# Kernel tuning notes

Hardware: AMD Instinct MI355X
Metric: run time of the kernel (lower is better)

The kernel has to match this reference:

```python
import jax, jax.numpy as jnp
import numpy as np

B, S, E, D, H = 4, 2048, 512, 64, 8
NEG = float(np.finfo(np.float64).min)  # tf uses tf.float64.min; overflows to -inf in fp32, same softmax effect


def setup_inputs() -> dict:
    key = jax.random.key(0)
    ks = jax.random.split(key, 6)
    std = 0.05  # tf.random_normal_initializer default stddev
    x = jax.random.normal(ks[0], (B, S, E), dtype=jnp.float32)
    Wq = jax.random.normal(ks[1], (H, E, D), dtype=jnp.float32) * std
    Wk = jax.random.normal(ks[2], (H, E, D), dtype=jnp.float32) * std
    Wvd = jax.random.normal(ks[3], (H, E, D), dtype=jnp.float32) * std
    Wvu = jax.random.normal(ks[4], (H, D, E), dtype=jnp.float32) * std
    Wo = jax.random.normal(ks[5], (H, 1), dtype=jnp.float32) * std
    return {"x": x, "Wq": Wq, "Wk": Wk, "Wvd": Wvd, "Wvu": Wvu, "Wo": Wo}


def reference(x, Wq, Wk, Wvd, Wvu, Wo):
    # Per-head projections, vectorized over the head axis h
    Q = jnp.einsum("bse,hed->bhsd", x, Wq)  # [B,H,S,D]
    K = jnp.einsum("bse,hed->bhsd", x, Wk)
    score = jnp.einsum("bhsd,bhtd->bhst", Q, K) / jnp.sqrt(jnp.float32(D))
    # tf.linalg.band_part(score, -1, 0): keep lower triangle (causal)
    tril = jnp.tril(jnp.ones((S, S), dtype=bool))
    score = jnp.where(tril, score, 0.0)
    # tf.where(score != 0, score, float64.min): masks zeros (incl. any exact-zero kept entries)
    score = jnp.where(score != 0, score, jnp.float32(NEG))
    attn = jax.nn.softmax(score, axis=-1)  # [B,H,S,S]
    # low-rank value projection: x @ (Wvdown @ Wvup) per head
    Wv = jnp.einsum("hed,hdf->hef", Wvd, Wvu)  # [H,E,E]
    V = jnp.einsum("bse,hef->bhsf", x, Wv)      # [B,H,S,E]
    heads = jnp.einsum("bhst,bhte->bhse", attn, V)  # [B,H,S,E]
    # stack on last axis then matmul with Wo[H,1] == weighted sum over heads
    out = jnp.einsum("bhse,h->bse", heads, Wo[:, 0])
    return out
```

## Files before the change

### kernel.cpp

```cpp
#include <hip/hip_runtime.h>
#include <math.h>
#include <type_traits>

namespace {
constexpr int B = 4, S = 2048, E = 512, D = 64, H = 8;
constexpr int KD = 512;

typedef short bf8 __attribute__((ext_vector_type(8)));
typedef short bf4 __attribute__((ext_vector_type(4)));
typedef float f4 __attribute__((ext_vector_type(4)));

__device__ __forceinline__ short f2bf(float f) {
  union { float f; unsigned u; } v; v.f = f;
  const unsigned r = v.u + 0x7fffu + ((v.u >> 16) & 1u);
  return (short)(r >> 16);
}

__device__ __forceinline__ unsigned cvt_pk_bf16(float a, float b) {
  unsigned r;
  asm("v_cvt_pk_bf16_f32 %0, %1, %2" : "=v"(r) : "v"(a), "v"(b));
  return r;
}

__device__ __forceinline__ void gload16(const void* g, void* l) {
  __builtin_amdgcn_global_load_lds(
      (const __attribute__((address_space(1))) unsigned int*)g,
      (__attribute__((address_space(3))) unsigned int*)l, 16, 0, 0);
}

__global__ __launch_bounds__(256) void prep_kernel(
    const float* __restrict__ x, const float* __restrict__ Wq,
    const float* __restrict__ Wk, const float* __restrict__ Wvd,
    const float* __restrict__ Wvu, const float* __restrict__ Wo,
    short* __restrict__ xb, short* __restrict__ WcatT,
    short* __restrict__ W2T) {
  __shared__ float T[64][65];
  const int bid = blockIdx.x;
  const int tid = threadIdx.x;
  if (bid < 2048) {
    const size_t i = ((size_t)bid * 256 + tid) * 8;
    const float4 v0 = *(const float4*)(x + i);
    const float4 v1 = *(const float4*)(x + i + 4);
    bf8 o;
    o[0] = f2bf(v0.x); o[1] = f2bf(v0.y); o[2] = f2bf(v0.z); o[3] = f2bf(v0.w);
    o[4] = f2bf(v1.x); o[5] = f2bf(v1.y); o[6] = f2bf(v1.z); o[7] = f2bf(v1.w);
    *(bf8*)(xb + i) = o;
  } else if (bid < 2240) {
    const int r = bid - 2048;
    const int cb = r >> 3, e0 = (r & 7) * 64;
    const int w = cb >> 3, h = cb & 7;
    const float* Wsel = (w == 0) ? Wq : (w == 1) ? Wk : Wvd;
    const float* Wp = Wsel + (size_t)h * E * D;
#pragma unroll
    for (int i = 0; i < 4; ++i) {
      const int f = tid + i * 256;
      const int rr = f >> 4, c4 = f & 15;
      const float4 v = *(const float4*)(Wp + (size_t)(e0 + rr) * D + c4 * 4);
      T[rr][c4 * 4 + 0] = v.x; T[rr][c4 * 4 + 1] = v.y;
      T[rr][c4 * 4 + 2] = v.z; T[rr][c4 * 4 + 3] = v.w;
    }
    __syncthreads();
#pragma unroll
    for (int i = 0; i < 4; ++i) {
      const int f = tid + i * 256;
      const int dr = f >> 4, e4 = f & 15;
      bf4 o;
#pragma unroll
      for (int j = 0; j < 4; ++j) o[j] = f2bf(T[e4 * 4 + j][dr]);
      *(bf4*)(WcatT + (size_t)(cb * 64 + dr) * KD + e0 + e4 * 4) = o;
    }
  } else {
    const int r = bid - 2240;
    const int h = r >> 3, e0 = (r & 7) * 64;
    const float wo = Wo[h];
#pragma unroll
    for (int i = 0; i < 4; ++i) {
      const int f = tid + i * 256;
      const int rr = f >> 4, c4 = f & 15;
      const float4 v = *(const float4*)(Wvu + ((size_t)h * D + rr) * E + e0 + c4 * 4);
      T[rr][c4 * 4 + 0] = v.x * wo; T[rr][c4 * 4 + 1] = v.y * wo;
      T[rr][c4 * 4 + 2] = v.z * wo; T[rr][c4 * 4 + 3] = v.w * wo;
    }
    __syncthreads();
#pragma unroll
    for (int i = 0; i < 4; ++i) {
      const int f = tid + i * 256;
      const int er = f >> 4, d4 = f & 15;
      bf4 o;
#pragma unroll
      for (int j = 0; j < 4; ++j) o[j] = f2bf(T[d4 * 4 + j][er]);
      *(bf4*)(W2T + (size_t)(e0 + er) * KD + h * 64 + d4 * 4) = o;
    }
  }
}

template <int MODE>
__global__ __launch_bounds__(256) void gemm_kernel(
    const short* __restrict__ A, const short* __restrict__ Bt,
    short* __restrict__ Qb, short* __restrict__ Kb, short* __restrict__ Vtg,
    float* __restrict__ Of) {
  const int row0 = blockIdx.x * 128;
  const int ct = blockIdx.y;
  const int tid = threadIdx.x;
  const int w = tid >> 6, l = tid & 63;
  const int wm = w >> 1, wn = w & 1;
  const int lr = l & 15, hi = l >> 4;

  __shared__ short As[128 * 64];
  __shared__ short Bs[128 * 64];

  const short* Ag = A + (size_t)row0 * KD;
  const short* Bg = Bt + (size_t)ct * 128 * KD;

  f4 acc[4][4] = {};
  for (int k0 = 0; k0 < KD; k0 += 64) {
    __syncthreads();
#pragma unroll
    for (int i = 0; i < 4; ++i) {
      const int f = i * 256 + tid;
      const int r = f >> 3, g = f & 7;
      gload16(Ag + (size_t)r * KD + k0 + ((g ^ (r & 7)) << 3), &As[f * 8]);
    }
#pragma unroll
    for (int i = 0; i < 4; ++i) {
      const int f = i * 256 + tid;
      const int r = f >> 3, g = f & 7;
      gload16(Bg + (size_t)r * KD + k0 + ((g ^ (r & 7)) << 3), &Bs[f * 8]);
    }
    __syncthreads();

    bf8 af[4][2], bfv[4][2];
#pragma unroll
    for (int t = 0; t < 4; ++t) {
#pragma unroll
      for (int kh = 0; kh < 2; ++kh) {
        const int ar = wm * 64 + t * 16 + lr;
        af[t][kh] = *(const bf8*)&As[ar * 64 + (((kh * 4 + hi) ^ (ar & 7)) << 3)];
        const int br = wn * 64 + t * 16 + lr;
        bfv[t][kh] = *(const bf8*)&Bs[br * 64 + (((kh * 4 + hi) ^ (br & 7)) << 3)];
      }
    }
#pragma unroll
    for (int mt = 0; mt < 4; ++mt)
#pragma unroll
      for (int nt = 0; nt < 4; ++nt) {
        acc[mt][nt] =
            __builtin_amdgcn_mfma_f32_16x16x32_bf16(af[mt][0], bfv[nt][0], acc[mt][nt], 0, 0, 0);
        acc[mt][nt] =
            __builtin_amdgcn_mfma_f32_16x16x32_bf16(af[mt][1], bfv[nt][1], acc[mt][nt], 0, 0, 0);
      }
  }

  if constexpr (MODE == 0) {
#pragma unroll
    for (int nt = 0; nt < 4; ++nt) {
      const int gc = ct * 128 + wn * 64 + nt * 16 + lr;
      const int cb = gc >> 6, d = gc & 63;
      const int h = cb & 7;
      if (cb < 16) {
        short* Out = (cb < 8) ? Qb : Kb;
#pragma unroll
        for (int mt = 0; mt < 4; ++mt)
#pragma unroll
          for (int reg = 0; reg < 4; ++reg) {
            const int grow = row0 + wm * 64 + mt * 16 + hi * 4 + reg;
            const int b = grow >> 11, s = grow & (S - 1);
            Out[(((size_t)(b * H + h) * S + s) << 6) + d] = f2bf(acc[mt][nt][reg]);
          }
      } else {
#pragma unroll
        for (int mt = 0; mt < 4; ++mt) {
          const int grow0 = row0 + wm * 64 + mt * 16 + hi * 4;
          const int b = grow0 >> 11, s0 = grow0 & (S - 1);
          bf4 o;
#pragma unroll
          for (int reg = 0; reg < 4; ++reg) o[reg] = f2bf(acc[mt][nt][reg]);
          *(bf4*)(Vtg + (((size_t)(b * H + h) * D + d) << 11) + s0) = o;
        }
      }
    }
  } else {
#pragma unroll
    for (int mt = 0; mt < 4; ++mt)
#pragma unroll
      for (int reg = 0; reg < 4; ++reg) {
        const int grow = row0 + wm * 64 + mt * 16 + hi * 4 + reg;
        float* orow = Of + (size_t)grow * 512 + ct * 128 + wn * 64;
#pragma unroll
        for (int nt = 0; nt < 4; ++nt) orow[nt * 16 + lr] = acc[mt][nt][reg];
      }
  }
}

__global__ __launch_bounds__(256) void attn_kernel(
    const short* __restrict__ Qb, const short* __restrict__ Kb,
    const short* __restrict__ Vt, short* __restrict__ PVb) {
  const int bh = blockIdx.x;
  const int qt = (int)(gridDim.y - 1 - blockIdx.y);
  const int b = bh >> 3, h = bh & 7;
  const int tid = threadIdx.x;
  const int w = tid >> 6, l = tid & 63;
  const int lr = l & 15, hi = l >> 4;

  __shared__ short KsA[64 * 64];
  __shared__ short KsB[64 * 64];
  __shared__ short VsA[64 * 64];
  __shared__ short VsB[64 * 64];

  const short* Qg = Qb + ((size_t)bh * S + qt * 64 + w * 16 + lr) * D;
  const bf8 qf0 = *(const bf8*)(Qg + hi * 8);
  const bf8 qf1 = *(const bf8*)(Qg + 32 + hi * 8);

  const short* Kg = Kb + (size_t)bh * S * D;
  const short* Vg = Vt + (size_t)bh * D * S;

  const int sr = tid >> 3, sg = tid & 7;
  const int sswz = (sg ^ (sr & 7)) << 3;
  const int sr2 = sr + 32, sswz2 = (sg ^ (sr2 & 7)) << 3;

  const short* kg0 = Kg + (size_t)sr * D + sswz;
  const short* kg1 = Kg + (size_t)sr2 * D + sswz2;
  const short* vg0 = Vg + (size_t)sr * S + sswz;
  const short* vg1 = Vg + (size_t)sr2 * S + sswz2;

  float lsum4[4] = {};
  f4 accO[4] = {};

  constexpr float LOG2E = 1.44269504088896340736f;
  constexpr float C1 = 0.125f * LOG2E;
  constexpr float C0 = -12.0f * LOG2E;

  auto step = [&](const short* Kl, const short* Vl, auto diag_c) {
    constexpr bool DIAG = decltype(diag_c)::value;
    f4 accS[4] = {};
    __builtin_amdgcn_s_setprio(1);
#pragma unroll
    for (int n = 0; n < 4; ++n) {
      const int tr = n * 16 + lr;
      const bf8 k0 = *(const bf8*)&Kl[tr * 64 + ((hi ^ (tr & 7)) << 3)];
      const bf8 k1 = *(const bf8*)&Kl[tr * 64 + (((4 + hi) ^ (tr & 7)) << 3)];
      accS[n] = __builtin_amdgcn_mfma_f32_16x16x32_bf16(k0, qf0, accS[n], 0, 0, 0);
      accS[n] = __builtin_amdgcn_mfma_f32_16x16x32_bf16(k1, qf1, accS[n], 0, 0, 0);
    }
    __builtin_amdgcn_s_setprio(0);

    bf4 pa[4];
#pragma unroll
    for (int n = 0; n < 4; ++n) {
      float p[4];
#pragma unroll
      for (int reg = 0; reg < 4; ++reg) {
        const float sv = accS[n][reg];
        bool ok = (sv != 0.f);
        if constexpr (DIAG) ok = ok && (n * 16 + hi * 4 + reg <= w * 16 + lr);
        p[reg] = ok ? exp2f(fmaf(sv, C1, C0)) : 0.f;
        lsum4[reg] += p[reg];
      }
      union { int2 i; bf4 v; } u;
      u.i.x = (int)cvt_pk_bf16(p[0], p[1]);
      u.i.y = (int)cvt_pk_bf16(p[2], p[3]);
      pa[n] = u.v;
    }

    __builtin_amdgcn_s_setprio(1);
#pragma unroll
    for (int np = 0; np < 4; ++np) {
      const int gb = 2 * np + (hi >> 1);
      const int ho = (hi & 1) << 2;
#pragma unroll
      for (int ne = 0; ne < 4; ++ne) {
        const int er = ne * 16 + lr;
        const bf4 vf = *(const bf4*)&Vl[er * 64 + ((gb ^ (er & 7)) << 3) + ho];
        accO[ne] = __builtin_amdgcn_mfma_f32_16x16x16bf16_1k(pa[np], vf, accO[ne], 0, 0, 0);
      }
    }
    __builtin_amdgcn_s_setprio(0);
  };

  gload16(kg0, &KsA[tid * 8]);
  gload16(kg1, &KsA[(256 + tid) * 8]);
  gload16(vg0, &VsA[tid * 8]);
  gload16(vg1, &VsA[(256 + tid) * 8]);
  kg0 += 64 * D; kg1 += 64 * D; vg0 += 64; vg1 += 64;

  short* Kc = KsA; short* Vc = VsA;
  short* Kn = KsB; short* Vn = VsB;

  for (int kt = 0; kt <= qt; ++kt) {
    if (kt > 0) {
      __builtin_amdgcn_s_barrier();
      __builtin_amdgcn_sched_barrier(0);
    }
    if (kt < qt) {
      gload16(kg0, &Kn[tid * 8]);
      gload16(kg1, &Kn[(256 + tid) * 8]);
      gload16(vg0, &Vn[tid * 8]);
      gload16(vg1, &Vn[(256 + tid) * 8]);
      kg0 += 64 * D; kg1 += 64 * D; vg0 += 64; vg1 += 64;
      asm volatile("s_waitcnt vmcnt(4)" ::: "memory");
    } else {
      asm volatile("s_waitcnt vmcnt(0)" ::: "memory");
    }
    __builtin_amdgcn_sched_barrier(0);
    __builtin_amdgcn_s_barrier();
    __builtin_amdgcn_sched_barrier(0);

    if (kt < qt) {
      step(Kc, Vc, std::integral_constant<bool, false>{});
    } else {
      step(Kc, Vc, std::integral_constant<bool, true>{});
    }
    { short* t = Kc; Kc = Kn; Kn = t; t = Vc; Vc = Vn; Vn = t; }
  }

  float lv = (lsum4[0] + lsum4[1]) + (lsum4[2] + lsum4[3]);
  lv += __shfl_xor(lv, 16);
  lv += __shfl_xor(lv, 32);
#pragma unroll
  for (int reg = 0; reg < 4; ++reg) {
    const float lq = __shfl(lv, hi * 4 + reg);
    const float inv = 1.f / lq;
    const int s = qt * 64 + w * 16 + hi * 4 + reg;
    short* op = PVb + (size_t)(b * S + s) * (H * D) + h * D;
#pragma unroll
    for (int n = 0; n < 4; ++n) op[n * 16 + lr] = f2bf(accO[n][reg] * inv);
  }
}

}

extern "C" void kernel_launch(void* const* d_in, const int* in_sizes, int n_in,
                              void* d_out, int out_size, void* d_ws, size_t ws_size,
                              hipStream_t stream) {
  const float* x   = (const float*)d_in[0];
  const float* Wq  = (const float*)d_in[1];
  const float* Wk  = (const float*)d_in[2];
  const float* Wvd = (const float*)d_in[3];
  const float* Wvu = (const float*)d_in[4];
  const float* Wo  = (const float*)d_in[5];
  float* out = (float*)d_out;

  const size_t nqk = (size_t)B * H * S * D;
  short* xb    = (short*)d_ws;
  short* Qb    = xb + nqk;
  short* Kb    = Qb + nqk;
  short* Vtg   = Kb + nqk;
  short* PVb   = Vtg + nqk;
  short* WcatT = PVb + nqk;
  short* W2T   = WcatT + 1536 * KD;

  prep_kernel<<<dim3(2304), 256, 0, stream>>>(x, Wq, Wk, Wvd, Wvu, Wo,
                                              xb, WcatT, W2T);
  gemm_kernel<0><<<dim3(64, 12), 256, 0, stream>>>(xb, WcatT, Qb, Kb, Vtg, nullptr);
  attn_kernel<<<dim3(B * H, S / 64), 256, 0, stream>>>(Qb, Kb, Vtg, PVb);
  gemm_kernel<1><<<dim3(64, 4), 256, 0, stream>>>(PVb, W2T, nullptr, nullptr, nullptr, out);
}
```

Before: 85.15 us.

## Pair causal query tiles per block and precompute swizzled LDS addresses

Each attention block now handles two query tiles (j and 31-j), so every block does a constant 33 key-tile steps and the grid halves. This balances the triangular causal workload and cuts launch tail imbalance. The V transpose store is XOR-swizzled by a nibble so the precomputed LDS byte offsets line up. The s!=0 mask is dropped in favour of the diagonal mask alone, and exp2 is replaced with __expf. Dropping the mask changes semantics if any score is exactly zero, and halving the block count may reduce occupancy.

```diff
diff --git a/kernel.cpp b/kernel.cpp
--- a/kernel.cpp
+++ b/kernel.cpp
@@ -168,10 +168,11 @@
             Out[(((size_t)(b * H + h) * S + s) << 6) + d] = f2bf(acc[mt][nt][reg]);
           }
       } else {
+        const int hswap = ((d >> 3) & 1) << 2;
 #pragma unroll
         for (int mt = 0; mt < 4; ++mt) {
           const int grow0 = row0 + wm * 64 + mt * 16 + hi * 4;
-          const int b = grow0 >> 11, s0 = grow0 & (S - 1);
+          const int b = grow0 >> 11, s0 = (grow0 & (S - 1)) ^ hswap;
           bf4 o;
 #pragma unroll
           for (int reg = 0; reg < 4; ++reg) o[reg] = f2bf(acc[mt][nt][reg]);
@@ -196,20 +197,23 @@
     const short* __restrict__ Qb, const short* __restrict__ Kb,
     const short* __restrict__ Vt, short* __restrict__ PVb) {
   const int bh = blockIdx.x;
-  const int qt = (int)(gridDim.y - 1 - blockIdx.y);
+  const int j = blockIdx.y;
+  const int qtA = j, qtB = 31 - j;
+  const int nA = j + 1;
   const int b = bh >> 3, h = bh & 7;
   const int tid = threadIdx.x;
   const int w = tid >> 6, l = tid & 63;
   const int lr = l & 15, hi = l >> 4;
 
-  __shared__ short KsA[64 * 64];
-  __shared__ short KsB[64 * 64];
-  __shared__ short VsA[64 * 64];
-  __shared__ short VsB[64 * 64];
-
-  const short* Qg = Qb + ((size_t)bh * S + qt * 64 + w * 16 + lr) * D;
-  const bf8 qf0 = *(const bf8*)(Qg + hi * 8);
-  const bf8 qf1 = *(const bf8*)(Qg + 32 + hi * 8);
+  __shared__ short Ks[2][64 * 64];
+  __shared__ short Vs[2][64 * 64];
+
+  const short* QgA = Qb + ((size_t)bh * S + qtA * 64 + w * 16 + lr) * D;
+  const short* QgB = Qb + ((size_t)bh * S + qtB * 64 + w * 16 + lr) * D;
+  const bf8 qA0 = *(const bf8*)(QgA + hi * 8);
+  const bf8 qA1 = *(const bf8*)(QgA + 32 + hi * 8);
+  const bf8 qB0 = *(const bf8*)(QgB + hi * 8);
+  const bf8 qB1 = *(const bf8*)(QgB + 32 + hi * 8);
 
   const short* Kg = Kb + (size_t)bh * S * D;
   const short* Vg = Vt + (size_t)bh * D * S;
@@ -217,30 +221,36 @@
   const int sr = tid >> 3, sg = tid & 7;
   const int sswz = (sg ^ (sr & 7)) << 3;
   const int sr2 = sr + 32, sswz2 = (sg ^ (sr2 & 7)) << 3;
-
   const short* kg0 = Kg + (size_t)sr * D + sswz;
   const short* kg1 = Kg + (size_t)sr2 * D + sswz2;
   const short* vg0 = Vg + (size_t)sr * S + sswz;
   const short* vg1 = Vg + (size_t)sr2 * S + sswz2;
 
+  const int e7 = lr & 7;
+  const int kla0 = lr * 128 + ((hi ^ e7) << 4);
+  const int kla1 = kla0 ^ 64;
+  const int x7 = (hi >> 1) ^ e7;
+  const int swaph = ((hi & 1) ^ ((lr >> 3) & 1)) << 3;
+  int vla[4];
+#pragma unroll
+  for (int np = 0; np < 4; ++np)
+    vla[np] = lr * 128 + (((2 * np) ^ x7) << 4) + swaph;
+
   float lsum4[4] = {};
   f4 accO[4] = {};
 
-  constexpr float LOG2E = 1.44269504088896340736f;
-  constexpr float C1 = 0.125f * LOG2E;
-  constexpr float C0 = -12.0f * LOG2E;
-
-  auto step = [&](const short* Kl, const short* Vl, auto diag_c) {
+  auto step = [&](int buf, bf8 q0, bf8 q1, auto diag_c) {
     constexpr bool DIAG = decltype(diag_c)::value;
+    const char* Klb = (const char*)Ks[buf];
+    const char* Vlb = (const char*)Vs[buf];
     f4 accS[4] = {};
     __builtin_amdgcn_s_setprio(1);
 #pragma unroll
     for (int n = 0; n < 4; ++n) {
-      const int tr = n * 16 + lr;
-      const bf8 k0 = *(const bf8*)&Kl[tr * 64 + ((hi ^ (tr & 7)) << 3)];
-      const bf8 k1 = *(const bf8*)&Kl[tr * 64 + (((4 + hi) ^ (tr & 7)) << 3)];
-      accS[n] = __builtin_amdgcn_mfma_f32_16x16x32_bf16(k0, qf0, accS[n], 0, 0, 0);
-      accS[n] = __builtin_amdgcn_mfma_f32_16x16x32_bf16(k1, qf1, accS[n], 0, 0, 0);
+      const bf8 k0 = *(const bf8*)(Klb + kla0 + n * 2048);
+      const bf8 k1 = *(const bf8*)(Klb + kla1 + n * 2048);
+      accS[n] = __builtin_amdgcn_mfma_f32_16x16x32_bf16(k0, q0, accS[n], 0, 0, 0);
+      accS[n] = __builtin_amdgcn_mfma_f32_16x16x32_bf16(k1, q1, accS[n], 0, 0, 0);
     }
     __builtin_amdgcn_s_setprio(0);
 
@@ -250,11 +260,13 @@
       float p[4];
 #pragma unroll
       for (int reg = 0; reg < 4; ++reg) {
-        const float sv = accS[n][reg];
-        bool ok = (sv != 0.f);
-        if constexpr (DIAG) ok = ok && (n * 16 + hi * 4 + reg <= w * 16 + lr);
-        p[reg] = ok ? exp2f(fmaf(sv, C1, C0)) : 0.f;
-        lsum4[reg] += p[reg];
+        float pv = __expf(fmaf(accS[n][reg], 0.125f, -12.0f));
+        if constexpr (DIAG) {
+          const bool ok = (n * 16 + hi * 4 + reg) <= (w * 16 + lr);
+          pv = ok ? pv : 0.f;
+        }
+        p[reg] = pv;
+        lsum4[reg] += pv;
       }
       union { int2 i; bf4 v; } u;
       u.i.x = (int)cvt_pk_bf16(p[0], p[1]);
@@ -265,38 +277,50 @@
     __builtin_amdgcn_s_setprio(1);
 #pragma unroll
     for (int np = 0; np < 4; ++np) {
-      const int gb = 2 * np + (hi >> 1);
-      const int ho = (hi & 1) << 2;
 #pragma unroll
       for (int ne = 0; ne < 4; ++ne) {
-        const int er = ne * 16 + lr;
-        const bf4 vf = *(const bf4*)&Vl[er * 64 + ((gb ^ (er & 7)) << 3) + ho];
+        const bf4 vf = *(const bf4*)(Vlb + vla[np] + ne * 2048);
         accO[ne] = __builtin_amdgcn_mfma_f32_16x16x16bf16_1k(pa[np], vf, accO[ne], 0, 0, 0);
       }
     }
     __builtin_amdgcn_s_setprio(0);
   };
 
-  gload16(kg0, &KsA[tid * 8]);
-  gload16(kg1, &KsA[(256 + tid) * 8]);
-  gload16(vg0, &VsA[tid * 8]);
-  gload16(vg1, &VsA[(256 + tid) * 8]);
-  kg0 += 64 * D; kg1 += 64 * D; vg0 += 64; vg1 += 64;
-
-  short* Kc = KsA; short* Vc = VsA;
-  short* Kn = KsB; short* Vn = VsB;
-
-  for (int kt = 0; kt <= qt; ++kt) {
-    if (kt > 0) {
+  auto epi = [&](int qt) {
+    float lv = (lsum4[0] + lsum4[1]) + (lsum4[2] + lsum4[3]);
+    lv += __shfl_xor(lv, 16);
+    lv += __shfl_xor(lv, 32);
+#pragma unroll
+    for (int reg = 0; reg < 4; ++reg) {
+      const float lq = __shfl(lv, hi * 4 + reg);
+      const float inv = 1.f / lq;
+      const int s = qt * 64 + w * 16 + hi * 4 + reg;
+      short* op = PVb + (size_t)(b * S + s) * (H * D) + h * D;
+#pragma unroll
+      for (int n = 0; n < 4; ++n) op[n * 16 + lr] = f2bf(accO[n][reg] * inv);
+    }
+  };
+
+  gload16(kg0, &Ks[0][tid * 8]);
+  gload16(kg1, &Ks[0][(256 + tid) * 8]);
+  gload16(vg0, &Vs[0][tid * 8]);
+  gload16(vg1, &Vs[0][(256 + tid) * 8]);
+
+  int buf = 0;
+  for (int s = 0; s < 33; ++s) {
+    if (s > 0) {
       __builtin_amdgcn_s_barrier();
       __builtin_amdgcn_sched_barrier(0);
     }
-    if (kt < qt) {
-      gload16(kg0, &Kn[tid * 8]);
-      gload16(kg1, &Kn[(256 + tid) * 8]);
-      gload16(vg0, &Vn[tid * 8]);
-      gload16(vg1, &Vn[(256 + tid) * 8]);
-      kg0 += 64 * D; kg1 += 64 * D; vg0 += 64; vg1 += 64;
+    if (s < 32) {
+      const int ktn = (s + 1 < nA) ? s + 1 : s + 1 - nA;
+      const size_t ko = (size_t)ktn << 12;
+      const size_t vo = (size_t)ktn << 6;
+      const int nb = buf ^ 1;
+      gload16(kg0 + ko, &Ks[nb][tid * 8]);
+      gload16(kg1 + ko, &Ks[nb][(256 + tid) * 8]);
+      gload16(vg0 + vo, &Vs[nb][tid * 8]);
+      gload16(vg1 + vo, &Vs[nb][(256 + tid) * 8]);
       asm volatile("s_waitcnt vmcnt(4)" ::: "memory");
     } else {
       asm volatile("s_waitcnt vmcnt(0)" ::: "memory");
@@ -305,26 +329,23 @@
     __builtin_amdgcn_s_barrier();
     __builtin_amdgcn_sched_barrier(0);
 
-    if (kt < qt) {
-      step(Kc, Vc, std::integral_constant<bool, false>{});
+    if (s < nA) {
+      if (s == nA - 1) step(buf, qA0, qA1, std::true_type{});
+      else             step(buf, qA0, qA1, std::false_type{});
     } else {
-      step(Kc, Vc, std::integral_constant<bool, true>{});
-    }
-    { short* t = Kc; Kc = Kn; Kn = t; t = Vc; Vc = Vn; Vn = t; }
+      if (s == 32)     step(buf, qB0, qB1, std::true_type{});
+      else             step(buf, qB0, qB1, std::false_type{});
+    }
+
+    if (s == nA - 1) {
+      epi(qtA);
+#pragma unroll
+      for (int n = 0; n < 4; ++n) accO[n] = f4{0.f, 0.f, 0.f, 0.f};
+      lsum4[0] = lsum4[1] = lsum4[2] = lsum4[3] = 0.f;
+    }
+    buf ^= 1;
   }
-
-  float lv = (lsum4[0] + lsum4[1]) + (lsum4[2] + lsum4[3]);
-  lv += __shfl_xor(lv, 16);
-  lv += __shfl_xor(lv, 32);
-#pragma unroll
-  for (int reg = 0; reg < 4; ++reg) {
-    const float lq = __shfl(lv, hi * 4 + reg);
-    const float inv = 1.f / lq;
-    const int s = qt * 64 + w * 16 + hi * 4 + reg;
-    short* op = PVb + (size_t)(b * S + s) * (H * D) + h * D;
-#pragma unroll
-    for (int n = 0; n < 4; ++n) op[n * 16 + lr] = f2bf(accO[n][reg] * inv);
-  }
+  epi(qtB);
 }
 
 }
@@ -352,6 +373,6 @@
   prep_kernel<<<dim3(2304), 256, 0, stream>>>(x, Wq, Wk, Wvd, Wvu, Wo,
                                               xb, WcatT, W2T);
   gemm_kernel<0><<<dim3(64, 12), 256, 0, stream>>>(xb, WcatT, Qb, Kb, Vtg, nullptr);
-  attn_kernel<<<dim3(B * H, S / 64), 256, 0, stream>>>(Qb, Kb, Vtg, PVb);
+  attn_kernel<<<dim3(B * H, 16), 256, 0, stream>>>(Qb, Kb, Vtg, PVb);
   gemm_kernel<1><<<dim3(64, 4), 256, 0, stream>>>(PVb, W2T, nullptr, nullptr, nullptr, out);
 }
```

Result: faster. 81.05 us (-4.8%).
